# Kernel tuning notes

Measured on AMD Instinct MI355X. Metric: run time of the kernel, lower is better.

Reference implementation:

```python
import jax, jax.numpy as jnp
import numpy as np

B, N, C_S, C_Z, C, H, PQ, PV = 1, 512, 384, 128, 16, 12, 4, 8
N_BLOCKS = 8
SCALE, EPS, INF = 10.0, 1e-8, 1e5
N_RESTYPES = 5
CAT = H * C + 4 * H * PV + H * C_Z  # IPA output concat width = 2112


def layer_norm(x, g, b):
    mu = jnp.mean(x, -1, keepdims=True)
    var = jnp.mean(jnp.square(x - mu), -1, keepdims=True)
    return (x - mu) * jax.lax.rsqrt(var + 1e-5) * g + b


def quat_mul(q, p):
    w1, x1, y1, z1 = q[..., 0], q[..., 1], q[..., 2], q[..., 3]
    w2, x2, y2, z2 = p[..., 0], p[..., 1], p[..., 2], p[..., 3]
    return jnp.stack([
        w1 * w2 - x1 * x2 - y1 * y2 - z1 * z2,
        w1 * x2 + x1 * w2 + y1 * z2 - z1 * y2,
        w1 * y2 - x1 * z2 + y1 * w2 + z1 * x2,
        w1 * z2 + x1 * y2 - y1 * x2 + z1 * w2], -1)


def quat_to_rot(q):
    w, x, y, z = q[..., 0], q[..., 1], q[..., 2], q[..., 3]
    r0 = jnp.stack([w * w + x * x - y * y - z * z, 2 * (x * y - w * z), 2 * (x * z + w * y)], -1)
    r1 = jnp.stack([2 * (x * y + w * z), w * w - x * x + y * y - z * z, 2 * (y * z - w * x)], -1)
    r2 = jnp.stack([2 * (x * z - w * y), 2 * (y * z + w * x), w * w - x * x - y * y + z * z], -1)
    return jnp.stack([r0, r1, r2], -2)  # [..., 3, 3]


def _forward(single, pair, restype, mask,
             ln_s_g, ln_s_b, ln_z_g, ln_z_b, w_in, b_in,
             wq, bq, wkv, bkv, wqp, bqp, wkvp, bkvp, wb, bb_z, head_w, wo, bo,
             ln_ipa_g, ln_ipa_b, t_w1, t_b1, t_w2, t_b2, t_w3, t_b3, ln_t_g, ln_t_b,
             w_bb, b_bb, lit_pos):
    Bv, Nv = single.shape[0], single.shape[1]
    s = layer_norm(single, ln_s_g, ln_s_b)
    z = layer_norm(pair, ln_z_g, ln_z_b)
    s = s @ w_in + b_in
    quats = jnp.zeros((Bv, Nv, 4), s.dtype).at[..., 0].set(1.0)  # identity rigid, quat fmt
    trans = jnp.zeros((Bv, Nv, 3), s.dtype)
    mask_bias = INF * (mask[..., :, None] * mask[..., None, :] - 1.0)  # [B,N,N]
    hw = jax.nn.softplus(head_w) * np.float32(np.sqrt(1.0 / (3.0 * (PQ * 9.0 / 2.0))))
    zb = jnp.transpose(z @ wb + bb_z, (0, 3, 1, 2))  # [B,H,N,N] pair bias, same each block
    lit = lit_pos[restype]  # [B,N,3atoms,3] literature backbone coords

    def run_ipa(s, rot, tr):
        q = (s @ wq + bq).reshape(Bv, Nv, H, C)
        kv = (s @ wkv + bkv).reshape(Bv, Nv, H, 2 * C)
        k, v = kv[..., :C], kv[..., C:]
        qp = (s @ wqp + bqp).reshape(Bv, Nv, 3, H * PQ).swapaxes(-1, -2)
        qp = (jnp.einsum('bnij,bnpj->bnpi', rot, qp) + tr[..., None, :]).reshape(Bv, Nv, H, PQ, 3)
        kvp = (s @ wkvp + bkvp).reshape(Bv, Nv, 3, H * (PQ + PV)).swapaxes(-1, -2)
        kvp = (jnp.einsum('bnij,bnpj->bnpi', rot, kvp) + tr[..., None, :]).reshape(Bv, Nv, H, PQ + PV, 3)
        kp, vp = kvp[..., :PQ, :], kvp[..., PQ:, :]
        a = jnp.einsum('bihc,bjhc->bhij', q, k) * np.float32(np.sqrt(1.0 / (3 * C)))
        a = a + np.float32(np.sqrt(1.0 / 3.0)) * zb
        d2 = jnp.sum(jnp.square(qp[:, :, None] - kp[:, None]), -1)  # [B,N,N,H,PQ]
        pt_att = -0.5 * jnp.sum(d2 * hw[:, None], -1)  # [B,N,N,H]
        a = jax.nn.softmax(a + jnp.transpose(pt_att, (0, 3, 1, 2)) + mask_bias[:, None], -1)
        o = jnp.einsum('bhij,bjhc->bihc', a, v).reshape(Bv, Nv, H * C)
        opt = jnp.einsum('bhij,bjhpx->bihpx', a, vp)  # attended points, global frame
        opt = jnp.einsum('bnji,bnhpj->bnhpi', rot, opt - tr[:, :, None, None, :])  # invert_apply
        opt_norm = jnp.sqrt(jnp.sum(jnp.square(opt), -1) + EPS).reshape(Bv, Nv, H * PV)
        opt_flat = jnp.moveaxis(opt.reshape(Bv, Nv, H * PV, 3), -1, -2).reshape(Bv, Nv, 3 * H * PV)
        opair = jnp.einsum('bhij,bijc->bihc', a, z).reshape(Bv, Nv, H * C_Z)
        return jnp.concatenate([o, opt_flat, opt_norm, opair], -1) @ wo + bo

    frames_l, pos_l, states_l = [], [], []
    for _ in range(N_BLOCKS):
        rot = quat_to_rot(quats)
        s = s + run_ipa(s, rot, trans)
        s = layer_norm(s, ln_ipa_g, ln_ipa_b)  # ipa dropout = identity (eval)
        t = jax.nn.relu(s @ t_w1 + t_b1)
        t = jax.nn.relu(t @ t_w2 + t_b2)
        s = layer_norm(s + t @ t_w3 + t_b3, ln_t_g, ln_t_b)  # transition (1 layer) + LN
        upd = s @ w_bb + b_bb  # [B,N,6] backbone update
        pq = jnp.concatenate([jnp.ones_like(upd[..., :1]), upd[..., :3]], -1)
        nq = quat_mul(quats, pq)
        quats = nq * jax.lax.rsqrt(jnp.sum(jnp.square(nq), -1, keepdims=True))
        trans = trans + jnp.einsum('bnij,bnj->bni', rot, upd[..., 3:])  # OLD rot applies t-update
        rot_new = quat_to_rot(quats)
        pos_l.append(jnp.einsum('bnij,bnaj->bnai', rot_new, lit) + SCALE * trans[..., None, :])
        frames_l.append(jnp.concatenate([quats, SCALE * trans], -1))
        states_l.append(s)
        quats = jax.lax.stop_gradient(quats)  # stop_rot_gradient
    return jnp.stack(frames_l), jnp.stack(pos_l), jnp.stack(states_l), s


def setup_inputs() -> dict:
    key = jax.random.key(0)
    ki = iter(jax.random.split(key, 48))
    def w(fan_in, fan_out):
        return jax.random.normal(next(ki), (fan_in, fan_out), jnp.float32) / np.sqrt(fan_in)
    inp = {
        "single": jax.random.normal(next(ki), (B, N, C_S), jnp.float32),
        "pair": jax.random.normal(next(ki), (B, N, N, C_Z), jnp.float32),
        "restype": jax.random.randint(next(ki), (B, N), 0, N_RESTYPES),
        "mask": jnp.ones((B, N), jnp.float32),
        "ln_s_g": jnp.ones((C_S,)), "ln_s_b": jnp.zeros((C_S,)),
        "ln_z_g": jnp.ones((C_Z,)), "ln_z_b": jnp.zeros((C_Z,)),
        "w_in": w(C_S, C_S), "b_in": jnp.zeros((C_S,)),
        "wq": w(C_S, H * C), "bq": jnp.zeros((H * C,)),
        "wkv": w(C_S, 2 * H * C), "bkv": jnp.zeros((2 * H * C,)),
        "wqp": w(C_S, H * PQ * 3), "bqp": jnp.zeros((H * PQ * 3,)),
        "wkvp": w(C_S, H * (PQ + PV) * 3), "bkvp": jnp.zeros((H * (PQ + PV) * 3,)),
        "wb": w(C_Z, H), "bb_z": jnp.zeros((H,)),
        "head_w": 0.1 * jax.random.normal(next(ki), (H,), jnp.float32),
        "wo": w(CAT, C_S), "bo": jnp.zeros((C_S,)),
        "ln_ipa_g": jnp.ones((C_S,)), "ln_ipa_b": jnp.zeros((C_S,)),
        "t_w1": w(C_S, C_S), "t_b1": jnp.zeros((C_S,)),
        "t_w2": w(C_S, C_S), "t_b2": jnp.zeros((C_S,)),
        "t_w3": w(C_S, C_S), "t_b3": jnp.zeros((C_S,)),
        "ln_t_g": jnp.ones((C_S,)), "ln_t_b": jnp.zeros((C_S,)),
        "w_bb": 0.001 * jax.random.normal(next(ki), (C_S, 6), jnp.float32),
        "b_bb": jnp.zeros((6,)),
        "lit_pos": jax.random.normal(next(ki), (N_RESTYPES, 3, 3), jnp.float32),
    }
    return inp


def reference(single, pair, restype, mask,
              ln_s_g, ln_s_b, ln_z_g, ln_z_b, w_in, b_in,
              wq, bq, wkv, bkv, wqp, bqp, wkvp, bkvp, wb, bb_z, head_w, wo, bo,
              ln_ipa_g, ln_ipa_b, t_w1, t_b1, t_w2, t_b2, t_w3, t_b3, ln_t_g, ln_t_b,
              w_bb, b_bb, lit_pos):
    return _forward(single, pair, restype, mask,
                    ln_s_g, ln_s_b, ln_z_g, ln_z_b, w_in, b_in,
                    wq, bq, wkv, bkv, wqp, bqp, wkvp, bkvp, wb, bb_z, head_w, wo, bo,
                    ln_ipa_g, ln_ipa_b, t_w1, t_b1, t_w2, t_b2, t_w3, t_b3, ln_t_g, ln_t_b,
                    w_bb, b_bb, lit_pos)
```

## Files before the change

### kernel.cpp

```cpp
#include <hip/hip_runtime.h>
#include <hip/hip_bf16.h>
#include <math.h>

typedef __hip_bfloat16 bf16;

#define DINL __device__ __forceinline__
DINL float b2f(bf16 x){ return __bfloat162float(x); }
DINL bf16 f2b(float x){ return __float2bfloat16(x); }

DINL float ldin(const void* p, size_t i, int isb){
    return isb ? b2f(((const bf16*)p)[i]) : ((const float*)p)[i];
}
DINL void stout(void* p, size_t i, float v, int isb){
    if(isb) ((bf16*)p)[i] = f2b(v); else ((float*)p)[i] = v;
}

static constexpr int NRES = 512;
static constexpr int CS   = 384;
static constexpr int CZ   = 128;
static constexpr int NH   = 12;
static constexpr int PQn  = 4;
static constexpr int CAT  = 2112;
static constexpr int ASTR = 516;
static constexpr int ZSTR = 136;
static constexpr int SAK  = 56;
static constexpr int KSTR = 40;
static constexpr int XSTR = 392;
static constexpr int PSPL = 4;
static constexpr int WSPL = 6;

typedef __attribute__((ext_vector_type(8))) short short8;
typedef __attribute__((ext_vector_type(4))) float f32x4;

__global__ void k_detect(const void* __restrict__ mask, int* __restrict__ flag){
    if(threadIdx.x==0 && blockIdx.x==0)
        flag[0] = (((const unsigned short*)mask)[0] == 0x3F80) ? 1 : 0;
}

#define MAXSEG 32
struct ConvSegs {
    const void* src[MAXSEG];
    int dst_off[MAXSEG];
    int blk0[MAXSEG];
    int total[MAXSEG];
};

__global__ void k_conv_multi(ConvSegs sg, int nseg, float* __restrict__ wsf,
                             const int* __restrict__ dt){
    int isb = dt[0];
    int b = blockIdx.x;
    int s = 0;
    #pragma unroll 1
    while(s+1 < nseg && sg.blk0[s+1] <= b) ++s;
    int idx = (b - sg.blk0[s])*256 + threadIdx.x;
    if(idx >= sg.total[s]) return;
    wsf[(size_t)sg.dst_off[s] + idx] = ldin(sg.src[s], idx, isb);
}

#define MAXTSEG 12
struct TSegs {
    const void* src[MAXTSEG];
    size_t dst_off[MAXTSEG];
    int N[MAXTSEG];
    int dstK[MAXTSEG];
    int blk0[MAXTSEG];
    int total[MAXTSEG];
};

__global__ void k_transpose_multi(TSegs sg, int nseg, bf16* __restrict__ base,
                                  const int* __restrict__ dt){
    int isb = dt[0];
    int b = blockIdx.x;
    int s = 0;
    #pragma unroll 1
    while(s+1 < nseg && sg.blk0[s+1] <= b) ++s;
    int idx = (b - sg.blk0[s])*256 + threadIdx.x;
    if(idx >= sg.total[s]) return;
    int N = sg.N[s];
    int k = idx / N, n = idx - k*N;
    base[sg.dst_off[s] + (size_t)n*sg.dstK[s] + k] = f2b(ldin(sg.src[s], idx, isb));
}

__global__ __launch_bounds__(128) void k_ln(const void* __restrict__ in, int in_dyn,
                     float* __restrict__ out, bf16* __restrict__ out16,
                     const float* __restrict__ g, const float* __restrict__ b, int Cdim,
                     const int* __restrict__ dt, int init_frames,
                     float* __restrict__ quats, float* __restrict__ trans){
    int row = blockIdx.x, tid = threadIdx.x;
    int isb = dt[0];
    int isb_in = in_dyn ? isb : 0;
    if(init_frames && tid==0){
        quats[row*4+0]=1.f; quats[row*4+1]=0.f; quats[row*4+2]=0.f; quats[row*4+3]=0.f;
        trans[row*3+0]=0.f; trans[row*3+1]=0.f; trans[row*3+2]=0.f;
    }
    float s=0.f, s2=0.f, vals[3];
    int r=0;
    for(int c=tid; c<Cdim; c+=128, ++r){
        size_t idx = (size_t)row*Cdim + c;
        float v = ldin(in, idx, isb_in);
        vals[r]=v; s+=v; s2+=v*v;
    }
    __shared__ float red[128], red2[128];
    red[tid]=s; red2[tid]=s2; __syncthreads();
    for(int st=64; st>0; st>>=1){ if(tid<st){ red[tid]+=red[tid+st]; red2[tid]+=red2[tid+st]; } __syncthreads(); }
    float mu = red[0]/Cdim;
    float var = red2[0]/Cdim - mu*mu;
    float rs = rsqrtf(var + 1e-5f);
    r=0;
    for(int c=tid; c<Cdim; c+=128, ++r){
        float v = (vals[r]-mu)*rs*g[c] + b[c];
        size_t idx = (size_t)row*Cdim + c;
        if(out)   out[idx] = v;
        if(out16) out16[idx] = f2b(v);
    }
}

__global__ __launch_bounds__(512) void k_mlp(
        const float* __restrict__ pw, const float* __restrict__ bo_f,
        float* __restrict__ s, bf16* __restrict__ s16,
        const float* __restrict__ lnig, const float* __restrict__ lnib,
        const bf16* __restrict__ tw1T, const float* __restrict__ tb1f,
        const bf16* __restrict__ tw2T, const float* __restrict__ tb2f,
        const bf16* __restrict__ tw3T, const float* __restrict__ tb3f,
        const float* __restrict__ lntg, const float* __restrict__ lntb,
        void* __restrict__ outp, size_t st_ofs, size_t fin_ofs, int mode,
        const int* __restrict__ dt,
        const float* __restrict__ wbb_f, const float* __restrict__ bbb_f,
        const float* __restrict__ rotp, const int* __restrict__ restype,
        const float* __restrict__ lit_f,
        float* __restrict__ quats, float* __restrict__ trans,
        size_t frames_ofs, size_t pos_ofs){
    __shared__ float sip[4*CS];
    __shared__ bf16  xa[16*XSTR];
    int t = threadIdx.x;
    int w = t>>6, lane = t&63;
    int quad = lane>>4, m16 = lane&15;
    int b0 = blockIdx.x*4;
    int isb = dt[0];

    if(w < 4){
        int r = w, gr = b0+r;
        float v[6];
        float sum=0.f, sq=0.f;
        #pragma unroll
        for(int kk=0;kk<6;kk++){
            int c = lane + kk*64;
            size_t idx = (size_t)gr*CS + c;
            float x = bo_f[c] + s[idx];
            #pragma unroll
            for(int p=0;p<WSPL;p++) x += pw[(size_t)p*NRES*CS + idx];
            v[kk]=x; sum+=x; sq+=x*x;
        }
        #pragma unroll
        for(int m=32;m>=1;m>>=1){ sum+=__shfl_xor(sum,m,64); sq+=__shfl_xor(sq,m,64); }
        float mu = sum*(1.f/CS);
        float rs = rsqrtf(sq*(1.f/CS) - mu*mu + 1e-5f);
        #pragma unroll
        for(int kk=0;kk<6;kk++){
            int c = lane + kk*64;
            float x = (v[kk]-mu)*rs*lnig[c] + lnib[c];
            sip[r*CS+c] = x;
            xa[r*XSTR+c] = f2b(x);
        }
    }
    __syncthreads();

    #pragma unroll
    for(int L=0; L<3; ++L){
        const bf16* WT   = (L==0) ? tw1T : (L==1) ? tw2T : tw3T;
        const float* bias= (L==0) ? tb1f : (L==1) ? tb2f : tb3f;
        const short* wt  = (const short*)WT;
        int nb = w*3;
        const short* wp0 = wt + (size_t)((nb+0)*16+m16)*CS + quad*8;
        const short* wp1 = wt + (size_t)((nb+1)*16+m16)*CS + quad*8;
        const short* wp2 = wt + (size_t)((nb+2)*16+m16)*CS + quad*8;
        f32x4 acc[3] = {};
        short8 wbuf[2][3];
        wbuf[0][0] = *(const short8*)(wp0);
        wbuf[0][1] = *(const short8*)(wp1);
        wbuf[0][2] = *(const short8*)(wp2);
        wbuf[1][0] = *(const short8*)(wp0 + 32);
        wbuf[1][1] = *(const short8*)(wp1 + 32);
        wbuf[1][2] = *(const short8*)(wp2 + 32);
        #pragma unroll
        for(int k=0;k<12;k++){
            short8 a = *(const short8*)((const short*)xa + m16*XSTR + k*32 + quad*8);
            short8 c0 = wbuf[k&1][0], c1 = wbuf[k&1][1], c2 = wbuf[k&1][2];
            if(k<10){
                wbuf[k&1][0] = *(const short8*)(wp0 + (k+2)*32);
                wbuf[k&1][1] = *(const short8*)(wp1 + (k+2)*32);
                wbuf[k&1][2] = *(const short8*)(wp2 + (k+2)*32);
            }
            acc[0] = __builtin_amdgcn_mfma_f32_16x16x32_bf16(a, c0, acc[0], 0,0,0);
            acc[1] = __builtin_amdgcn_mfma_f32_16x16x32_bf16(a, c1, acc[1], 0,0,0);
            acc[2] = __builtin_amdgcn_mfma_f32_16x16x32_bf16(a, c2, acc[2], 0,0,0);
        }
        __syncthreads();
        if(quad == 0){
            if(L<2){
                #pragma unroll
                for(int nt=0;nt<3;nt++){
                    int col = (nb+nt)*16 + m16;
                    float bb = bias[col];
                    #pragma unroll
                    for(int r=0;r<4;r++){
                        xa[r*XSTR+col] = f2b(fmaxf(acc[nt][r] + bb, 0.f));
                    }
                }
            } else {
                #pragma unroll
                for(int nt=0;nt<3;nt++){
                    int col = (nb+nt)*16 + m16;
                    float bb = bias[col];
                    #pragma unroll
                    for(int r=0;r<4;r++){
                        sip[r*CS+col] += acc[nt][r] + bb;
                    }
                }
            }
        }
        __syncthreads();
    }

    if(w < 4){
        int r = w, gr = b0+r;
        float v[6], facc[6]={};
        float sum=0.f, sq=0.f;
        #pragma unroll
        for(int kk=0;kk<6;kk++){
            float x = sip[r*CS + lane + kk*64];
            v[kk]=x; sum+=x; sq+=x*x;
        }
        #pragma unroll
        for(int m=32;m>=1;m>>=1){ sum+=__shfl_xor(sum,m,64); sq+=__shfl_xor(sq,m,64); }
        float mu = sum*(1.f/CS);
        float rs = rsqrtf(sq*(1.f/CS) - mu*mu + 1e-5f);
        #pragma unroll
        for(int kk=0;kk<6;kk++){
            int c = lane + kk*64;
            size_t idx = (size_t)gr*CS + c;
            float x = (v[kk]-mu)*rs*lntg[c] + lntb[c];
            s[idx] = x; s16[idx] = f2b(x);
            stout(outp, st_ofs + idx, x, isb);
            if(mode == 2) stout(outp, fin_ofs + idx, x, isb);
            #pragma unroll
            for(int j=0;j<6;j++) facc[j] += x * wbb_f[c*6+j];
        }
        #pragma unroll
        for(int m=32;m>=1;m>>=1){
            #pragma unroll
            for(int j=0;j<6;j++) facc[j] += __shfl_xor(facc[j], m, 64);
        }
        if(lane==0){
            int i = gr;
            float u[6];
            #pragma unroll
            for(int j=0;j<6;j++) u[j] = facc[j] + bbb_f[j];
            float qw=quats[i*4], qx=quats[i*4+1], qy=quats[i*4+2], qz=quats[i*4+3];
            float nw = qw       - qx*u[0] - qy*u[1] - qz*u[2];
            float nx = qw*u[0] + qx       + qy*u[2] - qz*u[1];
            float ny = qw*u[1] - qx*u[2] + qy       + qz*u[0];
            float nz = qw*u[2] + qx*u[1] - qy*u[0] + qz;
            float rn = rsqrtf(nw*nw + nx*nx + ny*ny + nz*nz);
            nw*=rn; nx*=rn; ny*=rn; nz*=rn;
            quats[i*4]=nw; quats[i*4+1]=nx; quats[i*4+2]=ny; quats[i*4+3]=nz;
            const float* R = rotp + i*9;
            float tx = trans[i*3]   + R[0]*u[3]+R[1]*u[4]+R[2]*u[5];
            float ty = trans[i*3+1] + R[3]*u[3]+R[4]*u[4]+R[5]*u[5];
            float tz = trans[i*3+2] + R[6]*u[3]+R[7]*u[4]+R[8]*u[5];
            trans[i*3]=tx; trans[i*3+1]=ty; trans[i*3+2]=tz;
            size_t f = frames_ofs + (size_t)i*7;
            stout(outp, f+0, nw, isb); stout(outp, f+1, nx, isb);
            stout(outp, f+2, ny, isb); stout(outp, f+3, nz, isb);
            stout(outp, f+4, 10.f*tx, isb); stout(outp, f+5, 10.f*ty, isb); stout(outp, f+6, 10.f*tz, isb);
            float Rn[9];
            Rn[0]=nw*nw+nx*nx-ny*ny-nz*nz; Rn[1]=2.f*(nx*ny-nw*nz);       Rn[2]=2.f*(nx*nz+nw*ny);
            Rn[3]=2.f*(nx*ny+nw*nz);       Rn[4]=nw*nw-nx*nx+ny*ny-nz*nz; Rn[5]=2.f*(ny*nz-nw*nx);
            Rn[6]=2.f*(nx*nz-nw*ny);       Rn[7]=2.f*(ny*nz+nw*nx);       Rn[8]=nw*nw-nx*nx-ny*ny+nz*nz;
            int rt = restype[i];
            size_t po = pos_ofs + (size_t)i*9;
            #pragma unroll
            for(int a=0;a<3;a++){
                float lx=lit_f[(rt*3+a)*3+0], ly=lit_f[(rt*3+a)*3+1], lz=lit_f[(rt*3+a)*3+2];
                stout(outp, po+a*3+0, Rn[0]*lx + Rn[1]*ly + Rn[2]*lz + 10.f*tx, isb);
                stout(outp, po+a*3+1, Rn[3]*lx + Rn[4]*ly + Rn[5]*lz + 10.f*ty, isb);
                stout(outp, po+a*3+2, Rn[6]*lx + Rn[7]*ly + Rn[8]*lz + 10.f*tz, isb);
            }
        }
    }
}

__global__ __launch_bounds__(256) void k_gemm_bf(const bf16* __restrict__ A,
        const bf16* __restrict__ BT, float* __restrict__ Cf, bf16* __restrict__ C16,
        const float* __restrict__ bias, const float* __restrict__ res,
        int M, int Nn, int K, int relu, int lda){
    __shared__ bf16 As[64*SAK];
    __shared__ bf16 Bs[64*SAK];
    int tid = threadIdx.x;
    int bm = blockIdx.y*64, bn = blockIdx.x*64;
    int kofs = blockIdx.z*K;
    int wave = tid>>6, lane = tid&63;
    int quad = lane>>4, m16 = lane&15;
    int wm = (wave>>1)*32, wn = (wave&1)*32;
    int srow = wave*16 + (lane>>2);
    int scol = (lane&3)*8;
    const bf16* Ag = A  + (size_t)(bm + srow)*lda + kofs + scol;
    const bf16* Bg = BT + (size_t)(bn + srow)*lda + kofs + scol;
    int ldw = srow*SAK + scol;
    f32x4 acc[2][2] = {};
    short8 ra = *(const short8*)Ag;
    short8 rb = *(const short8*)Bg;
    int nsteps = K >> 5;
    const short* Asp = (const short*)As;
    const short* Bsp = (const short*)Bs;
    for(int s=0; s<nsteps; ++s){
        __syncthreads();
        *(short8*)(As + ldw) = ra;
        *(short8*)(Bs + ldw) = rb;
        __syncthreads();
        if(s+1 < nsteps){
            ra = *(const short8*)(Ag + (size_t)(s+1)*32);
            rb = *(const short8*)(Bg + (size_t)(s+1)*32);
        }
        short8 a0 = *(const short8*)&Asp[(wm +      m16)*SAK + quad*8];
        short8 a1 = *(const short8*)&Asp[(wm + 16 + m16)*SAK + quad*8];
        short8 b0 = *(const short8*)&Bsp[(wn +      m16)*SAK + quad*8];
        short8 b1 = *(const short8*)&Bsp[(wn + 16 + m16)*SAK + quad*8];
        acc[0][0] = __builtin_amdgcn_mfma_f32_16x16x32_bf16(a0, b0, acc[0][0], 0,0,0);
        acc[0][1] = __builtin_amdgcn_mfma_f32_16x16x32_bf16(a0, b1, acc[0][1], 0,0,0);
        acc[1][0] = __builtin_amdgcn_mfma_f32_16x16x32_bf16(a1, b0, acc[1][0], 0,0,0);
        acc[1][1] = __builtin_amdgcn_mfma_f32_16x16x32_bf16(a1, b1, acc[1][1], 0,0,0);
    }
    float* Cfz = Cf ? Cf + (size_t)blockIdx.z*M*Nn : nullptr;
    #pragma unroll
    for(int tm=0;tm<2;tm++){
        #pragma unroll
        for(int r=0;r<4;r++){
            int row = bm + wm + tm*16 + quad*4 + r;
            #pragma unroll
            for(int tn=0;tn<2;tn++){
                int col = bn + wn + tn*16 + m16;
                float v = acc[tm][tn][r];
                if(bias) v += bias[col];
                if(res)  v += res[(size_t)row*Nn + col];
                if(relu) v = fmaxf(v, 0.f);
                if(Cfz) Cfz[(size_t)row*Nn + col] = v;
                if(C16) C16[(size_t)row*Nn + col] = f2b(v);
            }
        }
    }
}

__global__ __launch_bounds__(256) void k_zb_mfma(const void* __restrict__ pair,
        const float* __restrict__ gz, const float* __restrict__ bz,
        const bf16* __restrict__ wbT, bf16* __restrict__ zb16,
        bf16* __restrict__ zn16, const int* __restrict__ dt){
    int isb = dt[0];
    __shared__ float gs[CZ], bs[CZ];
    int t = threadIdx.x;
    if(t < CZ){ gs[t]=gz[t]; bs[t]=bz[t]; }
    int wave = t>>6, lane = t&63;
    int m = lane&15, quad = lane>>4;
    int r0 = blockIdx.x*128 + wave*32;
    const short* pps = (const short*)pair;
    const float* ppf = (const float*)pair;

    short8 bfrag[4];
    const short* wbs = (const short*)wbT;
    #pragma unroll
    for(int kc=0;kc<4;kc++) bfrag[kc] = *(const short8*)(wbs + m*CZ + kc*32 + quad*8);

    float vals0[32], vals1[32];
    if(isb){
        short8 pr0[4], pr1[4];
        const short* p0 = pps + (size_t)(r0 +      m)*CZ + quad*8;
        const short* p1 = pps + (size_t)(r0 + 16 + m)*CZ + quad*8;
        #pragma unroll
        for(int kc=0;kc<4;kc++) pr0[kc] = *(const short8*)(p0 + kc*32);
        #pragma unroll
        for(int kc=0;kc<4;kc++) pr1[kc] = *(const short8*)(p1 + kc*32);
        #pragma unroll
        for(int kc=0;kc<4;kc++)
            #pragma unroll
            for(int j=0;j<8;j++){
                vals0[kc*8+j] = b2f(((const bf16*)&pr0[kc])[j]);
                vals1[kc*8+j] = b2f(((const bf16*)&pr1[kc])[j]);
            }
    } else {
        const float* p0 = ppf + (size_t)(r0 +      m)*CZ + quad*8;
        const float* p1 = ppf + (size_t)(r0 + 16 + m)*CZ + quad*8;
        #pragma unroll
        for(int kc=0;kc<4;kc++){
            *(float4*)&vals0[kc*8]   = *(const float4*)(p0 + kc*32);
            *(float4*)&vals0[kc*8+4] = *(const float4*)(p0 + kc*32 + 4);
            *(float4*)&vals1[kc*8]   = *(const float4*)(p1 + kc*32);
            *(float4*)&vals1[kc*8+4] = *(const float4*)(p1 + kc*32 + 4);
        }
    }
    __syncthreads();

    #pragma unroll
    for(int tile=0; tile<2; ++tile){
        const float* vals = tile ? vals1 : vals0;
        int rowbase = r0 + tile*16;
        int row = rowbase + m;
        float s=0.f, s2=0.f;
        #pragma unroll
        for(int j=0;j<32;j++){ float v=vals[j]; s+=v; s2+=v*v; }
        s  += __shfl_xor(s,16,64);  s  += __shfl_xor(s,32,64);
        s2 += __shfl_xor(s2,16,64); s2 += __shfl_xor(s2,32,64);
        float mu = s*(1.f/CZ);
        float var = s2*(1.f/CZ) - mu*mu;
        float rsd = rsqrtf(var + 1e-5f);
        f32x4 acc = {0.f,0.f,0.f,0.f};
        #pragma unroll
        for(int kc=0;kc<4;kc++){
            int c0 = kc*32 + quad*8;
            short8 a;
            #pragma unroll
            for(int j=0;j<8;j++){
                float zn = (vals[kc*8+j]-mu)*rsd*gs[c0+j] + bs[c0+j];
                ((bf16*)&a)[j] = f2b(zn);
            }
            *(short8*)((short*)zn16 + (size_t)row*CZ + c0) = a;
            acc = __builtin_amdgcn_mfma_f32_16x16x32_bf16(a, bfrag[kc], acc, 0, 0, 0);
        }
        if(m < NH){
            unsigned short pk[4];
            #pragma unroll
            for(int r=0;r<4;r++){ bf16 h = f2b(acc[r]); pk[r] = *(unsigned short*)&h; }
            size_t o = (size_t)m*((size_t)NRES*NRES) + (size_t)(rowbase + quad*4);
            *(uint2*)((unsigned short*)zb16 + o) = *(const uint2*)pk;
        }
    }
}


__global__ __launch_bounds__(192) void k_rotate_kv(const float* __restrict__ qpw,
        const float* __restrict__ bproj,
        const float* __restrict__ quats, const float* __restrict__ trans,
        float* __restrict__ rot,
        float* __restrict__ qp_rot, float* __restrict__ kp_rot, bf16* __restrict__ vp16,
        float* __restrict__ k_buf, bf16* __restrict__ v16, float* __restrict__ q_buf){
    int i = blockIdx.x, t = threadIdx.x;
    __shared__ float R[9], T[3];
    __shared__ float rowbuf[1152];
    const float* qb = qpw + (size_t)i*1152;
    #pragma unroll
    for(int r=0;r<6;r++){
        int c = t + 192*r;
        float acc = bproj[c];
        #pragma unroll
        for(int p=0;p<PSPL;p++) acc += qb[(size_t)p*NRES*1152 + c];
        rowbuf[c] = acc;
    }
    if(t==0){
        float w=quats[i*4],x=quats[i*4+1],y=quats[i*4+2],z=quats[i*4+3];
        R[0]=w*w+x*x-y*y-z*z; R[1]=2.f*(x*y-w*z);     R[2]=2.f*(x*z+w*y);
        R[3]=2.f*(x*y+w*z);   R[4]=w*w-x*x+y*y-z*z;   R[5]=2.f*(y*z-w*x);
        R[6]=2.f*(x*z-w*y);   R[7]=2.f*(y*z+w*x);     R[8]=w*w-x*x-y*y+z*z;
    }
    if(t<3) T[t] = trans[i*3+t];
    __syncthreads();
    if(t<9) rot[i*9+t] = R[t];
    q_buf[(size_t)i*192 + t] = rowbuf[t];
    {
        int h = t/16, c = t%16;
        k_buf[((size_t)h*NRES + i)*16 + c] = rowbuf[192 + h*32 + c];
        v16[(size_t)i*192 + t]             = f2b(rowbuf[192 + h*32 + 16 + c]);
    }
    if(t < 48){
        float vx = rowbuf[576 + t], vy = rowbuf[576 + 48 + t], vz = rowbuf[576 + 96 + t];
        float* o = qp_rot + ((size_t)i*48 + t)*3;
        o[0] = R[0]*vx + R[1]*vy + R[2]*vz + T[0];
        o[1] = R[3]*vx + R[4]*vy + R[5]*vz + T[1];
        o[2] = R[6]*vx + R[7]*vy + R[8]*vz + T[2];
    }
    if(t < 144){
        int hp = t;
        float vx = rowbuf[720 + hp], vy = rowbuf[720 + 144 + hp], vz = rowbuf[720 + 288 + hp];
        float ox = R[0]*vx + R[1]*vy + R[2]*vz + T[0];
        float oy = R[3]*vx + R[4]*vy + R[5]*vz + T[1];
        float oz = R[6]*vx + R[7]*vy + R[8]*vz + T[2];
        int h = hp/12, p = hp%12;
        if(p < PQn){
            float* o = kp_rot + ((size_t)i*48 + h*4 + p)*3;
            o[0]=ox; o[1]=oy; o[2]=oz;
        } else {
            bf16* o = vp16 + ((size_t)i*96 + h*8 + (p-4))*3;
            o[0]=f2b(ox); o[1]=f2b(oy); o[2]=f2b(oz);
        }
    }
}

__global__ __launch_bounds__(256) void k_attn(const float* __restrict__ q_buf,
        const float* __restrict__ k_buf, const float* __restrict__ qp_rot,
        const float* __restrict__ kp_rot, const bf16* __restrict__ zb16,
        const float* __restrict__ hw_f, const float* __restrict__ bbz_f,
        const void* __restrict__ mask, bf16* __restrict__ a16,
        const int* __restrict__ dt){
    int i0 = blockIdx.x*16, h = blockIdx.y;
    int t = threadIdx.x;
    int isb = dt[0];
    __shared__ bf16 kb_s[NRES*KSTR];
    __shared__ bf16 zb_s[16*NRES];
    __shared__ bf16 as_s[16*KSTR];
    __shared__ float colc_s[NRES];
    __shared__ float mcol_s[NRES];
    __shared__ float rowc_s[16], mrow_s[16];
    __shared__ float redm[4][16], reds[4][16];
    float hwx = hw_f[h];
    float sp = (hwx > 20.f) ? hwx : log1pf(expf(hwx));
    float hw = sp * 0.13608276348795434f;
    float zbb = 0.57735026919f * bbz_f[h];
    #pragma unroll
    for(int rr=0; rr<2; ++rr){
        int j = t*2 + rr;
        const float* kr  = k_buf  + ((size_t)h*NRES + j)*16;
        const float* kpr = kp_rot + ((size_t)j*48 + h*4)*3;
        bf16* dstp = kb_s + j*KSTR;
        float kv[16], pv[12];
        *(float4*)&kv[0]  = *(const float4*)(kr);
        *(float4*)&kv[4]  = *(const float4*)(kr + 4);
        *(float4*)&kv[8]  = *(const float4*)(kr + 8);
        *(float4*)&kv[12] = *(const float4*)(kr + 12);
        *(float4*)&pv[0]  = *(const float4*)(kpr);
        *(float4*)&pv[4]  = *(const float4*)(kpr + 4);
        *(float4*)&pv[8]  = *(const float4*)(kpr + 8);
        #pragma unroll
        for(int c=0;c<16;c++) dstp[c] = f2b(kv[c]);
        float s2k = 0.f;
        #pragma unroll
        for(int p=0;p<12;p++){ float v = pv[p]; s2k += v*v; dstp[16+p] = f2b(v); }
        dstp[28]=f2b(0.f); dstp[29]=f2b(0.f); dstp[30]=f2b(0.f); dstp[31]=f2b(0.f);
        colc_s[j] = -0.5f*hw*s2k;
        mcol_s[j] = ldin(mask, j, isb);
    }
    {
        const short8* zsrc = (const short8*)((const unsigned short*)zb16 + (size_t)h*NRES*NRES + (size_t)i0*NRES);
        short8* zdst = (short8*)zb_s;
        #pragma unroll
        for(int r=0;r<4;r++) zdst[t + r*256] = zsrc[t + r*256];
    }
    if(t < 16){
        int m = t;
        const float* qr = q_buf + (size_t)(i0+m)*192 + h*16;
        bf16* dstp = as_s + m*KSTR;
        float qv[16], qpv[12];
        *(float4*)&qv[0]  = *(const float4*)(qr);
        *(float4*)&qv[4]  = *(const float4*)(qr + 4);
        *(float4*)&qv[8]  = *(const float4*)(qr + 8);
        *(float4*)&qv[12] = *(const float4*)(qr + 12);
        const float* qpr = qp_rot + ((size_t)(i0+m)*48 + h*4)*3;
        *(float4*)&qpv[0] = *(const float4*)(qpr);
        *(float4*)&qpv[4] = *(const float4*)(qpr + 4);
        *(float4*)&qpv[8] = *(const float4*)(qpr + 8);
        #pragma unroll
        for(int c=0;c<16;c++) dstp[c] = f2b(qv[c]*0.14433756729740643f);
        float s2q = 0.f;
        #pragma unroll
        for(int p=0;p<12;p++){ float v = qpv[p]; s2q += v*v; dstp[16+p] = f2b(v*hw); }
        dstp[28]=f2b(0.f); dstp[29]=f2b(0.f); dstp[30]=f2b(0.f); dstp[31]=f2b(0.f);
        rowc_s[m] = -0.5f*hw*s2q;
        mrow_s[m] = ldin(mask, i0+m, isb);
    }
    __syncthreads();
    int lane = t&63, wv = t>>6;
    int quad = lane>>4, m16 = lane&15;
    short8 afrag = *(const short8*)((const short*)as_s + m16*KSTR + quad*8);
    float l[8][4];
    #pragma unroll
    for(int tt=0; tt<8; ++tt){
        int jt = wv*8 + tt;
        short8 bfrag = *(const short8*)((const short*)kb_s + (jt*16+m16)*KSTR + quad*8);
        f32x4 acc = {0.f,0.f,0.f,0.f};
        acc = __builtin_amdgcn_mfma_f32_16x16x32_bf16(afrag, bfrag, acc, 0,0,0);
        int j = jt*16 + m16;
        float cc = colc_s[j] + zbb;
        float mj = mcol_s[j];
        #pragma unroll
        for(int r=0;r<4;r++){
            int row = quad*4 + r;
            float zbv = b2f(zb_s[row*NRES + j]);
            l[tt][r] = acc[r] + 0.57735026919f*zbv + cc + rowc_s[row]
                     + 100000.0f*(mrow_s[row]*mj - 1.0f);
        }
    }
    float lm[4], ls[4];
    #pragma unroll
    for(int r=0;r<4;r++){
        float m = l[0][r];
        #pragma unroll
        for(int tt=1;tt<8;tt++) m = fmaxf(m, l[tt][r]);
        #pragma unroll
        for(int msk=1; msk<16; msk<<=1) m = fmaxf(m, __shfl_xor(m, msk, 64));
        lm[r] = m;
        float s = 0.f;
        #pragma unroll
        for(int tt=0;tt<8;tt++){ float e = expf(l[tt][r]-m); l[tt][r] = e; s += e; }
        #pragma unroll
        for(int msk=1; msk<16; msk<<=1) s += __shfl_xor(s, msk, 64);
        ls[r] = s;
    }
    if(m16 == 0){
        #pragma unroll
        for(int r=0;r<4;r++){ redm[wv][quad*4+r] = lm[r]; reds[wv][quad*4+r] = ls[r]; }
    }
    __syncthreads();
    #pragma unroll
    for(int r=0;r<4;r++){
        int row = quad*4+r;
        float M = redm[0][row];
        #pragma unroll
        for(int w=1;w<4;w++) M = fmaxf(M, redm[w][row]);
        float S = 0.f;
        #pragma unroll
        for(int w=0;w<4;w++) S += reds[w][row]*expf(redm[w][row]-M);
        float f = expf(lm[r]-M)/S;
        #pragma unroll
        for(int tt=0;tt<8;tt++){
            int j = (wv*8+tt)*16 + m16;
            a16[((size_t)h*NRES + i0+row)*NRES + j] = f2b(l[tt][r]*f);
        }
    }
}

__global__ __launch_bounds__(512) void k_attn_out(const bf16* __restrict__ a16,
        const bf16* __restrict__ v16, const bf16* __restrict__ vp16,
        const bf16* __restrict__ zn16,
        const float* __restrict__ rot, const float* __restrict__ trans,
        bf16* __restrict__ o_cat16){
    int i = blockIdx.x, t = threadIdx.x;
    __shared__ float a_sf[NH*ASTR];
    __shared__ bf16  zn_s[32*ZSTR];
    __shared__ float opt_s[288];
    for(int vv=t; vv<768; vv+=512){
        int h = vv>>6, j8 = (vv&63)*8;
        short8 a8 = *(const short8*)((const short*)a16 + (size_t)h*NRES*NRES + (size_t)i*NRES + j8);
        float* dst = a_sf + h*ASTR + j8;
        #pragma unroll
        for(int u=0;u<8;u++) dst[u] = b2f(((const bf16*)&a8)[u]);
    }
    int lane = t&63, quad = lane>>4, m16 = lane&15;
    int wv = t>>6;
    int jj = t>>4, c8 = (t&15)*8;
    int pc = t;
    int h0 = (pc<192) ? (pc>>4) : (pc-192)/24;
    const bf16* s0 = (pc<192) ? (v16 + pc) : (vp16 + (pc-192));
    int st0 = (pc<192) ? 192 : 288;
    const bf16* s1 = vp16 + 192 + t;
    int h1 = (192 + t)/24;
    float acc0 = 0.f, acc1 = 0.f;
    f32x4 macc[4] = {};
    __syncthreads();
    for(int j0=0; j0<NRES; j0+=32){
        if(j0) __syncthreads();
        {
            size_t pb = ((size_t)i*NRES + j0+jj)*CZ + c8;
            short8 z8 = *(const short8*)((const short*)zn16 + pb);
            *(short8*)&zn_s[jj*ZSTR + c8] = z8;
        }
        __syncthreads();
        if(wv < 6){
            const float* ap0 = a_sf + h0*ASTR;
            #pragma unroll
            for(int u=0; u<32; u+=4){
                int j = j0+u;
                float4 a4 = *(const float4*)(ap0 + j);
                acc0 += a4.x*b2f(s0[(size_t)j*st0])     + a4.y*b2f(s0[(size_t)(j+1)*st0])
                      + a4.z*b2f(s0[(size_t)(j+2)*st0]) + a4.w*b2f(s0[(size_t)(j+3)*st0]);
            }
            if(t < 96){
                const float* ap1 = a_sf + h1*ASTR;
                #pragma unroll
                for(int u=0; u<32; u+=4){
                    int j = j0+u;
                    float4 a4 = *(const float4*)(ap1 + j);
                    acc1 += a4.x*b2f(s1[(size_t)j*288])     + a4.y*b2f(s1[(size_t)(j+1)*288])
                          + a4.z*b2f(s1[(size_t)(j+2)*288]) + a4.w*b2f(s1[(size_t)(j+3)*288]);
                }
            }
        } else {
            float4 af0 = *(const float4*)&a_sf[m16*ASTR + j0 + quad*8];
            float4 af1 = *(const float4*)&a_sf[m16*ASTR + j0 + quad*8 + 4];
            short8 afrag;
            float az[8] = {af0.x,af0.y,af0.z,af0.w,af1.x,af1.y,af1.z,af1.w};
            #pragma unroll
            for(int r=0;r<8;r++) ((bf16*)&afrag)[r] = f2b((m16 < NH) ? az[r] : 0.f);
            int cbase = (wv-6)*64;
            #pragma unroll
            for(int tn=0; tn<4; ++tn){
                int c0 = cbase + tn*16;
                short8 bfrag;
                #pragma unroll
                for(int r=0;r<8;r++) ((bf16*)&bfrag)[r] = zn_s[(quad*8+r)*ZSTR + c0 + m16];
                macc[tn] = __builtin_amdgcn_mfma_f32_16x16x32_bf16(afrag, bfrag, macc[tn], 0,0,0);
            }
        }
    }
    if(wv >= 6){
        int cbase = (wv-6)*64;
        #pragma unroll
        for(int tn=0; tn<4; ++tn){
            int c = cbase + tn*16 + m16;
            #pragma unroll
            for(int r=0;r<4;r++){
                int h = quad*4 + r;
                if(h < NH) o_cat16[(size_t)i*CAT + 576 + h*CZ + c] = f2b(macc[tn][r]);
            }
        }
    } else {
        if(pc < 192) o_cat16[(size_t)i*CAT + pc] = f2b(acc0);
        else         opt_s[pc-192] = acc0;
        if(t < 96)   opt_s[192+t] = acc1;
    }
    __syncthreads();
    if(t < 96){
        float R0=rot[i*9+0],R1=rot[i*9+1],R2=rot[i*9+2];
        float R3=rot[i*9+3],R4=rot[i*9+4],R5=rot[i*9+5];
        float R6=rot[i*9+6],R7=rot[i*9+7],R8=rot[i*9+8];
        float T0=trans[i*3+0],T1=trans[i*3+1],T2=trans[i*3+2];
        const float* v = opt_s + t*3;
        float vx=v[0]-T0, vy=v[1]-T1, vz=v[2]-T2;
        float ox = R0*vx + R3*vy + R6*vz;
        float oy = R1*vx + R4*vy + R7*vz;
        float oz = R2*vx + R5*vy + R8*vz;
        bf16* o = o_cat16 + (size_t)i*CAT;
        o[192 +       t] = f2b(ox);
        o[192 +  96 + t] = f2b(oy);
        o[192 + 192 + t] = f2b(oz);
        o[480 + t] = f2b(sqrtf(ox*ox + oy*oy + oz*oz + 1e-8f));
    }
}


extern "C" void kernel_launch(void* const* d_in, const int* in_sizes, int n_in,
                              void* d_out, int out_size, void* d_ws, size_t ws_size,
                              hipStream_t stream){
    (void)in_sizes; (void)n_in; (void)out_size; (void)ws_size;
    const void* single = d_in[0];
    const void* pair   = d_in[1];
    const int*  restype= (const int*)d_in[2];
    const void* mask   = d_in[3];

    float* wsf = (float*)d_ws;
    bf16*  wsb = (bf16*)d_ws;
    size_t off = 0;
    auto alloc  = [&](size_t n){ float* p = wsf + off; off += (n + 3) & ~(size_t)3; return p; };
    auto allocB = [&](size_t n){ bf16* p = (bf16*)(wsf + off); off += ((n+1)/2 + 3) & ~(size_t)3; return p; };
    int*   dflag  = (int*)alloc(4);
    float* s      = alloc((size_t)NRES*CS);
    float* pw     = alloc((size_t)WSPL*NRES*CS);
    float* qpw    = alloc((size_t)PSPL*NRES*1152);
    float* q_buf  = alloc((size_t)NRES*192);
    float* qp_rot = alloc((size_t)NRES*144);
    float* kp_rot = alloc((size_t)NRES*144);
    float* k_bufp = alloc((size_t)NH*NRES*16);
    float* quats  = alloc(NRES*4);
    float* trans  = alloc(NRES*3);
    float* rot    = alloc(NRES*9);
    bf16*  a16    = allocB((size_t)NH*NRES*NRES);
    bf16*  zb16   = allocB((size_t)NH*NRES*NRES);
    bf16*  zn16   = allocB((size_t)NRES*NRES*CZ);
    bf16*  v16    = allocB((size_t)NRES*192);
    bf16*  vp16   = allocB((size_t)NRES*288);
    bf16*  o_cat16= allocB((size_t)NRES*CAT);
    bf16*  sin16  = allocB((size_t)NRES*CS);
    bf16*  s16    = allocB((size_t)NRES*CS);
    bf16*  WprojT = allocB((size_t)1152*CS);
    bf16*  w_inT  = allocB((size_t)CS*CS);
    bf16*  woT    = allocB((size_t)CS*CAT);
    bf16*  tw1T   = allocB((size_t)CS*CS);
    bf16*  tw2T   = allocB((size_t)CS*CS);
    bf16*  tw3T   = allocB((size_t)CS*CS);
    bf16*  wbT    = allocB(16*CZ);
    float* b_in_f = alloc(CS);
    float* bproj  = alloc(1152);
    float* bo_f   = alloc(CS);
    float* tb1f   = alloc(CS);
    float* tb2f   = alloc(CS);
    float* tb3f   = alloc(CS);
    float* lnsg   = alloc(CS);
    float* lnsb   = alloc(CS);
    float* lnig   = alloc(CS);
    float* lnib   = alloc(CS);
    float* lntg   = alloc(CS);
    float* lntb   = alloc(CS);
    float* gz_f   = alloc(CZ);
    float* bz_f   = alloc(CZ);
    float* bbz_f  = alloc(16);
    float* hw_f   = alloc(16);
    float* wbb_f  = alloc(CS*6);
    float* bbb_f  = alloc(8);
    float* lit_f  = alloc(48);

    const size_t OF_FRAMES = 0;
    const size_t OF_POS    = 28672;
    const size_t OF_STATES = 65536;
    const size_t OF_FINAL  = 1638400;

    k_detect<<<1,64,0,stream>>>(mask, dflag);

    ConvSegs sg;
    int nseg = 0, blk = 0;
    auto plain = [&](const void* src, float* dst, int total){
        sg.src[nseg]=src; sg.dst_off[nseg]=(int)(dst - wsf);
        sg.total[nseg]=total; sg.blk0[nseg]=blk;
        blk += (total+255)/256; ++nseg;
    };
    plain(d_in[11], bproj,     192);
    plain(d_in[13], bproj+192, 384);
    plain(d_in[15], bproj+576, 144);
    plain(d_in[17], bproj+720, 432);
    plain(d_in[9],  b_in_f, CS);
    plain(d_in[22], bo_f,   CS);
    plain(d_in[26], tb1f,   CS);
    plain(d_in[28], tb2f,   CS);
    plain(d_in[30], tb3f,   CS);
    plain(d_in[4],  lnsg,   CS);
    plain(d_in[5],  lnsb,   CS);
    plain(d_in[23], lnig,   CS);
    plain(d_in[24], lnib,   CS);
    plain(d_in[31], lntg,   CS);
    plain(d_in[32], lntb,   CS);
    plain(d_in[6],  gz_f,   CZ);
    plain(d_in[7],  bz_f,   CZ);
    plain(d_in[19], bbz_f,  NH);
    plain(d_in[20], hw_f,   NH);
    plain(d_in[34], bbb_f,  6);
    plain(d_in[35], lit_f,  45);
    plain(d_in[33], wbb_f,  CS*6);
    k_conv_multi<<<blk,256,0,stream>>>(sg, nseg, wsf, dflag);

    TSegs tg;
    int ntseg = 0, tblk = 0;
    auto trs = [&](const void* src, int K, int N, bf16* dst, int rowofs, int dstK){
        tg.src[ntseg]=src;
        tg.dst_off[ntseg]=(size_t)(dst - wsb) + (size_t)rowofs*dstK;
        tg.N[ntseg]=N; tg.dstK[ntseg]=dstK;
        tg.total[ntseg]=K*N; tg.blk0[ntseg]=tblk;
        tblk += (K*N+255)/256; ++ntseg;
    };
    trs(d_in[10], CS, 192, WprojT, 0,   CS);
    trs(d_in[12], CS, 384, WprojT, 192, CS);
    trs(d_in[14], CS, 144, WprojT, 576, CS);
    trs(d_in[16], CS, 432, WprojT, 720, CS);
    trs(d_in[8],  CS, CS,  w_inT,  0,   CS);
    trs(d_in[21], CAT, CS, woT,    0,   CAT);
    trs(d_in[25], CS, CS,  tw1T,   0,   CS);
    trs(d_in[27], CS, CS,  tw2T,   0,   CS);
    trs(d_in[29], CS, CS,  tw3T,   0,   CS);
    trs(d_in[18], CZ, NH,  wbT,    0,   CZ);
    k_transpose_multi<<<tblk,256,0,stream>>>(tg, ntseg, wsb, dflag);

    k_zb_mfma<<<NRES*NRES/128,256,0,stream>>>(pair, gz_f, bz_f, wbT, zb16, zn16, dflag);

    k_ln<<<NRES,128,0,stream>>>(single, 1, nullptr, sin16, lnsg, lnsb, CS, dflag, 1, quats, trans);
    {
        dim3 g(CS/64, NRES/64);
        k_gemm_bf<<<g,256,0,stream>>>(sin16, w_inT, s, s16, b_in_f, nullptr, NRES, CS, CS, 0, CS);
    }

    for(int bi=0; bi<8; ++bi){
        {
            dim3 gp(1152/64, NRES/64, PSPL);
            k_gemm_bf<<<gp,256,0,stream>>>(s16, WprojT, qpw, nullptr, nullptr, nullptr,
                                           NRES, 1152, 384/PSPL, 0, CS);
        }
        k_rotate_kv<<<NRES,192,0,stream>>>(qpw, bproj, quats, trans, rot, qp_rot, kp_rot,
                                           vp16, k_bufp, v16, q_buf);
        {
            dim3 g(NRES/16, NH);
            k_attn<<<g,256,0,stream>>>(q_buf, k_bufp, qp_rot, kp_rot, zb16, hw_f, bbz_f, mask, a16, dflag);
        }
        k_attn_out<<<NRES,512,0,stream>>>(a16, v16, vp16, zn16, rot, trans, o_cat16);
        {
            dim3 gw(CS/64, NRES/64, WSPL);
            k_gemm_bf<<<gw,256,0,stream>>>(o_cat16, woT, pw, nullptr, nullptr, nullptr,
                                           NRES, CS, CAT/WSPL, 0, CAT);
            k_mlp<<<NRES/4,512,0,stream>>>(pw, bo_f, s, s16, lnig, lnib,
                                            tw1T, tb1f, tw2T, tb2f, tw3T, tb3f,
                                            lntg, lntb,
                                            d_out, OF_STATES + (size_t)bi*NRES*CS, OF_FINAL,
                                            (bi==7) ? 2 : 1, dflag,
                                            wbb_f, bbb_f, rot, restype, lit_f,
                                            quats, trans,
                                            OF_FRAMES + (size_t)bi*NRES*7,
                                            OF_POS + (size_t)bi*NRES*9);
        }
    }
}
```

Before: 1.276 ms.

## Coalesce pair loads in z-bias kernel via LDS staging of normalized rows

```diff
diff --git a/kernel.cpp b/kernel.cpp
--- a/kernel.cpp
+++ b/kernel.cpp
@@ -357,81 +357,105 @@
         bf16* __restrict__ zn16, const int* __restrict__ dt){
     int isb = dt[0];
     __shared__ float gs[CZ], bs[CZ];
+    __shared__ float rsum[64], rsq[64];
+    __shared__ float mu_s[64], rs_s[64];
+    __shared__ bf16 zn_s[64*ZSTR];
     int t = threadIdx.x;
     if(t < CZ){ gs[t]=gz[t]; bs[t]=bz[t]; }
+    size_t rbase = (size_t)blockIdx.x*64;
+    float xv[32];
+
+    if(isb){
+        const short8* src = (const short8*)((const short*)pair + rbase*CZ);
+        #pragma unroll
+        for(int r=0;r<4;r++){
+            short8 c = src[r*256 + t];
+            #pragma unroll
+            for(int j=0;j<8;j++) xv[r*8+j] = b2f(((const bf16*)&c)[j]);
+        }
+        #pragma unroll
+        for(int r=0;r<4;r++){
+            float s=0.f, s2=0.f;
+            #pragma unroll
+            for(int j=0;j<8;j++){ float v=xv[r*8+j]; s+=v; s2+=v*v; }
+            #pragma unroll
+            for(int m=1;m<16;m<<=1){ s+=__shfl_xor(s,m,64); s2+=__shfl_xor(s2,m,64); }
+            if((t&15)==0){ int row = r*16 + (t>>4); rsum[row]=s; rsq[row]=s2; }
+        }
+    } else {
+        const float4* src = (const float4*)((const float*)pair + rbase*CZ);
+        #pragma unroll
+        for(int r=0;r<8;r++){
+            float4 c = src[r*256 + t];
+            xv[r*4+0]=c.x; xv[r*4+1]=c.y; xv[r*4+2]=c.z; xv[r*4+3]=c.w;
+        }
+        #pragma unroll
+        for(int r=0;r<8;r++){
+            float s=0.f, s2=0.f;
+            #pragma unroll
+            for(int j=0;j<4;j++){ float v=xv[r*4+j]; s+=v; s2+=v*v; }
+            #pragma unroll
+            for(int m=1;m<32;m<<=1){ s+=__shfl_xor(s,m,64); s2+=__shfl_xor(s2,m,64); }
+            if((t&31)==0){ int row = r*8 + (t>>5); rsum[row]=s; rsq[row]=s2; }
+        }
+    }
+    __syncthreads();
+    if(t < 64){
+        float mu = rsum[t]*(1.f/CZ);
+        float var = rsq[t]*(1.f/CZ) - mu*mu;
+        mu_s[t] = mu; rs_s[t] = rsqrtf(var + 1e-5f);
+    }
+    __syncthreads();
+
+    if(isb){
+        #pragma unroll
+        for(int r=0;r<4;r++){
+            int row = r*16 + (t>>4);
+            int c0  = (t&15)*8;
+            float mu = mu_s[row], rs = rs_s[row];
+            short8 o;
+            #pragma unroll
+            for(int j=0;j<8;j++)
+                ((bf16*)&o)[j] = f2b((xv[r*8+j]-mu)*rs*gs[c0+j] + bs[c0+j]);
+            *(short8*)&zn_s[row*ZSTR + c0] = o;
+            *(short8*)((short*)zn16 + (rbase+row)*CZ + c0) = o;
+        }
+    } else {
+        #pragma unroll
+        for(int r=0;r<8;r++){
+            int row = r*8 + (t>>5);
+            int c0  = (t&31)*4;
+            float mu = mu_s[row], rs = rs_s[row];
+            unsigned short pk[4];
+            #pragma unroll
+            for(int j=0;j<4;j++){
+                bf16 h = f2b((xv[r*4+j]-mu)*rs*gs[c0+j] + bs[c0+j]);
+                pk[j] = *(unsigned short*)&h;
+                zn_s[row*ZSTR + c0 + j] = h;
+            }
+            *(uint2*)((unsigned short*)zn16 + (rbase+row)*CZ + c0) = *(const uint2*)pk;
+        }
+    }
+    __syncthreads();
+
     int wave = t>>6, lane = t&63;
     int m = lane&15, quad = lane>>4;
-    int r0 = blockIdx.x*128 + wave*32;
-    const short* pps = (const short*)pair;
-    const float* ppf = (const float*)pair;
-
     short8 bfrag[4];
     const short* wbs = (const short*)wbT;
     #pragma unroll
     for(int kc=0;kc<4;kc++) bfrag[kc] = *(const short8*)(wbs + m*CZ + kc*32 + quad*8);
-
-    float vals0[32], vals1[32];
-    if(isb){
-        short8 pr0[4], pr1[4];
-        const short* p0 = pps + (size_t)(r0 +      m)*CZ + quad*8;
-        const short* p1 = pps + (size_t)(r0 + 16 + m)*CZ + quad*8;
-        #pragma unroll
-        for(int kc=0;kc<4;kc++) pr0[kc] = *(const short8*)(p0 + kc*32);
-        #pragma unroll
-        for(int kc=0;kc<4;kc++) pr1[kc] = *(const short8*)(p1 + kc*32);
-        #pragma unroll
-        for(int kc=0;kc<4;kc++)
-            #pragma unroll
-            for(int j=0;j<8;j++){
-                vals0[kc*8+j] = b2f(((const bf16*)&pr0[kc])[j]);
-                vals1[kc*8+j] = b2f(((const bf16*)&pr1[kc])[j]);
-            }
-    } else {
-        const float* p0 = ppf + (size_t)(r0 +      m)*CZ + quad*8;
-        const float* p1 = ppf + (size_t)(r0 + 16 + m)*CZ + quad*8;
-        #pragma unroll
-        for(int kc=0;kc<4;kc++){
-            *(float4*)&vals0[kc*8]   = *(const float4*)(p0 + kc*32);
-            *(float4*)&vals0[kc*8+4] = *(const float4*)(p0 + kc*32 + 4);
-            *(float4*)&vals1[kc*8]   = *(const float4*)(p1 + kc*32);
-            *(float4*)&vals1[kc*8+4] = *(const float4*)(p1 + kc*32 + 4);
-        }
-    }
-    __syncthreads();
-
+    f32x4 acc = {0.f,0.f,0.f,0.f};
     #pragma unroll
-    for(int tile=0; tile<2; ++tile){
-        const float* vals = tile ? vals1 : vals0;
-        int rowbase = r0 + tile*16;
-        int row = rowbase + m;
-        float s=0.f, s2=0.f;
-        #pragma unroll
-        for(int j=0;j<32;j++){ float v=vals[j]; s+=v; s2+=v*v; }
-        s  += __shfl_xor(s,16,64);  s  += __shfl_xor(s,32,64);
-        s2 += __shfl_xor(s2,16,64); s2 += __shfl_xor(s2,32,64);
-        float mu = s*(1.f/CZ);
-        float var = s2*(1.f/CZ) - mu*mu;
-        float rsd = rsqrtf(var + 1e-5f);
-        f32x4 acc = {0.f,0.f,0.f,0.f};
-        #pragma unroll
-        for(int kc=0;kc<4;kc++){
-            int c0 = kc*32 + quad*8;
-            short8 a;
-            #pragma unroll
-            for(int j=0;j<8;j++){
-                float zn = (vals[kc*8+j]-mu)*rsd*gs[c0+j] + bs[c0+j];
-                ((bf16*)&a)[j] = f2b(zn);
-            }
-            *(short8*)((short*)zn16 + (size_t)row*CZ + c0) = a;
-            acc = __builtin_amdgcn_mfma_f32_16x16x32_bf16(a, bfrag[kc], acc, 0, 0, 0);
-        }
-        if(m < NH){
-            unsigned short pk[4];
-            #pragma unroll
-            for(int r=0;r<4;r++){ bf16 h = f2b(acc[r]); pk[r] = *(unsigned short*)&h; }
-            size_t o = (size_t)m*((size_t)NRES*NRES) + (size_t)(rowbase + quad*4);
-            *(uint2*)((unsigned short*)zb16 + o) = *(const uint2*)pk;
-        }
+    for(int kc=0;kc<4;kc++){
+        short8 a = *(const short8*)((const short*)zn_s + (wave*16+m)*ZSTR + kc*32 + quad*8);
+        acc = __builtin_amdgcn_mfma_f32_16x16x32_bf16(a, bfrag[kc], acc, 0, 0, 0);
+    }
+    if(m < NH){
+        unsigned short pk[4];
+        #pragma unroll
+        for(int r=0;r<4;r++){ bf16 h = f2b(acc[r]); pk[r] = *(unsigned short*)&h; }
+        size_t o = (size_t)m*((size_t)NRES*NRES) + rbase + wave*16 + quad*4;
+        *(uint2*)((unsigned short*)zb16 + o) = *(const uint2*)pk;
     }
 }
 
@@ -853,7 +877,7 @@
     trs(d_in[18], CZ, NH,  wbT,    0,   CZ);
     k_transpose_multi<<<tblk,256,0,stream>>>(tg, ntseg, wsb, dflag);
 
-    k_zb_mfma<<<NRES*NRES/128,256,0,stream>>>(pair, gz_f, bz_f, wbT, zb16, zn16, dflag);
+    k_zb_mfma<<<NRES*NRES/64,256,0,stream>>>(pair, gz_f, bz_f, wbT, zb16, zn16, dflag);
 
     k_ln<<<NRES,128,0,stream>>>(single, 1, nullptr, sin16, lnsg, lnsb, CS, dflag, 1, quats, trans);
     {
```

Result: no change. 1.272 ms (-0.4%).
